# Kernel tuning notes

Hardware: AMD Instinct MI355X
Metric: run time of the kernel (lower is better)

The kernel has to match this reference:

```python
import jax, jax.numpy as jnp
import numpy as np

N, E, DIN, DOUT = 100000, 1200000, 64, 64


def setup_inputs() -> dict:
    key = jax.random.key(0)
    ks = jax.random.split(key, 6)
    x = jax.random.normal(ks[0], (N, DIN), dtype=jnp.float32)
    edge_index = jax.random.randint(ks[1], (2, E), 0, N, dtype=jnp.int32)
    edge_weight = jax.random.uniform(ks[2], (E,), dtype=jnp.float32)
    # msg_mlp: Linear(in_dim, out_dim) + ReLU
    W_msg = jax.random.normal(ks[3], (DIN, DOUT), dtype=jnp.float32) / np.sqrt(DIN)
    b_msg = jnp.zeros((DOUT,), dtype=jnp.float32)
    # update_fn (concat): Linear(in_dim + out_dim, out_dim) + ReLU
    W_upd = jax.random.normal(ks[4], (DIN + DOUT, DOUT), dtype=jnp.float32) / np.sqrt(DIN + DOUT)
    b_upd = jnp.zeros((DOUT,), dtype=jnp.float32)
    return {"x": x, "edge_index": edge_index, "edge_weight": edge_weight,
            "W_msg": W_msg, "b_msg": b_msg, "W_upd": W_upd, "b_upd": b_upd}


def reference(x, edge_index, edge_weight, W_msg, b_msg, W_upd, b_upd):
    src_idx, dst_idx = edge_index[0], edge_index[1]
    num_nodes = x.shape[0]
    # gather source node features, apply Linear+ReLU, scale by edge weight
    src_feat = x[src_idx]                                  # [E, DIN]
    msg = jax.nn.relu(src_feat @ W_msg + b_msg)            # [E, DOUT]
    msg = msg * edge_weight[:, None]
    # mean aggregation: scatter-add then divide by clamped in-degree
    agg = jax.ops.segment_sum(msg, dst_idx, num_segments=num_nodes)   # [N, DOUT]
    deg = jax.ops.segment_sum(jnp.ones((msg.shape[0],), msg.dtype), dst_idx,
                              num_segments=num_nodes)
    agg = agg / jnp.maximum(deg, 1.0)[:, None]
    # concat combine: Linear([x || agg]) + ReLU
    h = jax.nn.relu(jnp.concatenate([x, agg], axis=1) @ W_upd + b_upd)  # [N, DOUT]
    # F.normalize(p=2, dim=1), eps=1e-12
    norm = jnp.sqrt(jnp.sum(h * h, axis=1, keepdims=True))
    return h / jnp.maximum(norm, 1e-12)
```

## Files before the change

### kernel.cpp

```cpp
#include <hip/hip_runtime.h>
#include <hip/hip_fp16.h>


#define DIM 64
#define NPB 1024
#define LOG_NPB 10
#define NBUCK_MAX 128
#define CAP 16384
#define CHUNK 2048
#define EPT 8

typedef _Float16 half8 __attribute__((ext_vector_type(8)));
typedef float f32x4 __attribute__((ext_vector_type(4)));

__global__ __launch_bounds__(256) void k_mfmaA(
    const float* __restrict__ x, const float* __restrict__ Wm,
    const float* __restrict__ bm, const float* __restrict__ Wu,
    const float* __restrict__ bu, __half* __restrict__ y,
    __half* __restrict__ tq, int n) {
  int l = threadIdx.x & 63;
  int wv = threadIdx.x >> 6;
  int r = l & 15, g = l >> 4;

  half8 Bm[2][4], Bu[2][4];
#pragma unroll
  for (int ks = 0; ks < 2; ++ks)
#pragma unroll
    for (int ct = 0; ct < 4; ++ct) {
      int c = ct * 16 + r;
#pragma unroll
      for (int j = 0; j < 8; ++j) {
        int k = ks * 32 + g * 8 + j;
        Bm[ks][ct][j] = (_Float16)Wm[k * 64 + c];
        Bu[ks][ct][j] = (_Float16)Wu[k * 64 + c];
      }
    }
  float bmv[4], buv[4];
#pragma unroll
  for (int ct = 0; ct < 4; ++ct) { bmv[ct] = bm[ct * 16 + r]; buv[ct] = bu[ct * 16 + r]; }

  int ntiles = (n + 15) >> 4;
  int tile = blockIdx.x * 4 + wv;
  if (tile >= ntiles) return;
  int row0 = tile << 4;

  int arow = row0 + r; if (arow >= n) arow = n - 1;
  const float* xr = x + (size_t)arow * 64;
  half8 A[2];
#pragma unroll
  for (int ks = 0; ks < 2; ++ks) {
    float4 v0 = *(const float4*)(xr + ks * 32 + g * 8);
    float4 v1 = *(const float4*)(xr + ks * 32 + g * 8 + 4);
    A[ks][0] = (_Float16)v0.x; A[ks][1] = (_Float16)v0.y;
    A[ks][2] = (_Float16)v0.z; A[ks][3] = (_Float16)v0.w;
    A[ks][4] = (_Float16)v1.x; A[ks][5] = (_Float16)v1.y;
    A[ks][6] = (_Float16)v1.z; A[ks][7] = (_Float16)v1.w;
  }

  f32x4 Dm[4], Du[4];
#pragma unroll
  for (int ct = 0; ct < 4; ++ct)
#pragma unroll
    for (int q = 0; q < 4; ++q) { Dm[ct][q] = bmv[ct]; Du[ct][q] = buv[ct]; }

#pragma unroll
  for (int ks = 0; ks < 2; ++ks)
#pragma unroll
    for (int ct = 0; ct < 4; ++ct) {
      Dm[ct] = __builtin_amdgcn_mfma_f32_16x16x32_f16(A[ks], Bm[ks][ct], Dm[ct], 0, 0, 0);
      Du[ct] = __builtin_amdgcn_mfma_f32_16x16x32_f16(A[ks], Bu[ks][ct], Du[ct], 0, 0, 0);
    }

#pragma unroll
  for (int q = 0; q < 4; ++q) {
    int row = row0 + g * 4 + q;
    if (row < n) {
#pragma unroll
      for (int ct = 0; ct < 4; ++ct) {
        y[(size_t)row * 64 + ct * 16 + r]  = __float2half(fmaxf(Dm[ct][q], 0.0f));
        tq[(size_t)row * 64 + ct * 16 + r] = __float2half(Du[ct][q]);
      }
    }
  }
}

__global__ __launch_bounds__(256) void k_partA(
    const int* __restrict__ src, const int* __restrict__ dst,
    const float* __restrict__ ew,
    unsigned long long* __restrict__ recS, unsigned short* __restrict__ dlocS,
    int* __restrict__ bucketCur, int E, int nbuck) {
  __shared__ int hist[NBUCK_MAX];
  __shared__ int gbase[NBUCK_MAX];
  int t = threadIdx.x;
  int base = blockIdx.x * CHUNK;

  for (int b = t; b < nbuck; b += 256) hist[b] = 0;
  __syncthreads();

  unsigned long long rec[EPT];
  unsigned short dl[EPT];
  short bk[EPT];
#pragma unroll
  for (int i = 0; i < EPT; ++i) {
    int e = base + i * 256 + t;
    if (e < E) {
      int d = dst[e];
      int b = d >> LOG_NPB;
      bk[i] = (short)b;
      dl[i] = (unsigned short)(d & (NPB - 1));
      rec[i] = ((unsigned long long)__float_as_uint(ew[e]) << 32) | (unsigned)src[e];
      atomicAdd(&hist[b], 1);
    } else {
      bk[i] = -1;
    }
  }
  __syncthreads();
  for (int b = t; b < nbuck; b += 256)
    gbase[b] = atomicAdd(&bucketCur[b], hist[b]);
  __syncthreads();
  for (int b = t; b < nbuck; b += 256) hist[b] = 0;
  __syncthreads();
#pragma unroll
  for (int i = 0; i < EPT; ++i) {
    if (bk[i] >= 0) {
      int b = bk[i];
      int lp = gbase[b] + atomicAdd(&hist[b], 1);
      if (lp < CAP) {
        size_t pos = (size_t)b * CAP + lp;
        recS[pos] = rec[i];
        dlocS[pos] = dl[i];
      }
    }
  }
}

__global__ __launch_bounds__(1024) void k_partB(
    const unsigned long long* __restrict__ recS, const unsigned short* __restrict__ dlocS,
    const int* __restrict__ bucketCur,
    unsigned long long* __restrict__ sw, int* __restrict__ cnt,
    int* __restrict__ rowstart, int n) {
  __shared__ int lcnt[NPB];
  __shared__ int loff[NPB];
  __shared__ int wsum[16];
  int b = blockIdx.x;
  int t = threadIdx.x;
  int m = bucketCur[b];
  if (m > CAP) m = CAP;
  size_t sbase = (size_t)b * CAP;
  int bktbase = 0;
  for (int q = 0; q < b; ++q) bktbase += bucketCur[q];

  lcnt[t] = 0;
  __syncthreads();
  for (int i = t; i < m; i += 1024)
    atomicAdd(&lcnt[dlocS[sbase + i]], 1);
  __syncthreads();

  int v = lcnt[t];
  int lane = t & 63;
  int incl = v;
#pragma unroll
  for (int off = 1; off < 64; off <<= 1) {
    int tt = __shfl_up(incl, off, 64);
    if (lane >= off) incl += tt;
  }
  if (lane == 63) wsum[t >> 6] = incl;
  __syncthreads();
  int woff = 0;
  for (int q = 0; q < (t >> 6); ++q) woff += wsum[q];
  int excl = incl - v + woff;
  loff[t] = excl;
  int gn = (b << LOG_NPB) + t;
  if (gn < n) {
    cnt[gn] = v;
    rowstart[gn] = bktbase + excl;
  }
  __syncthreads();

  for (int i = t; i < m; i += 1024) {
    int dl = dlocS[sbase + i];
    int p = atomicAdd(&loff[dl], 1);
    sw[bktbase + p] = recS[sbase + i];
  }
}

__global__ __launch_bounds__(256) void k_gather(
    const unsigned long long* __restrict__ sw, const int* __restrict__ rowstart,
    const int* __restrict__ cnt, const __half2* __restrict__ y2,
    float* __restrict__ agg, int n) {
  int lane = threadIdx.x & 31;
  int node = (int)((blockIdx.x * (size_t)blockDim.x + threadIdx.x) >> 5);
  if (node >= n) return;
  int c = cnt[node];
  int e = rowstart[node];
  int end = e + c;
  float ax = 0.0f, ay = 0.0f;
  for (; e + 8 <= end; e += 8) {
    unsigned long long r0 = sw[e + 0];
    unsigned long long r1 = sw[e + 1];
    unsigned long long r2 = sw[e + 2];
    unsigned long long r3 = sw[e + 3];
    unsigned long long r4 = sw[e + 4];
    unsigned long long r5 = sw[e + 5];
    unsigned long long r6 = sw[e + 6];
    unsigned long long r7 = sw[e + 7];
    __half2 v0 = y2[(size_t)(unsigned)(r0 & 0xFFFFFFFFu) * 32 + lane];
    __half2 v1 = y2[(size_t)(unsigned)(r1 & 0xFFFFFFFFu) * 32 + lane];
    __half2 v2 = y2[(size_t)(unsigned)(r2 & 0xFFFFFFFFu) * 32 + lane];
    __half2 v3 = y2[(size_t)(unsigned)(r3 & 0xFFFFFFFFu) * 32 + lane];
    __half2 v4 = y2[(size_t)(unsigned)(r4 & 0xFFFFFFFFu) * 32 + lane];
    __half2 v5 = y2[(size_t)(unsigned)(r5 & 0xFFFFFFFFu) * 32 + lane];
    __half2 v6 = y2[(size_t)(unsigned)(r6 & 0xFFFFFFFFu) * 32 + lane];
    __half2 v7 = y2[(size_t)(unsigned)(r7 & 0xFFFFFFFFu) * 32 + lane];
    float w0 = __uint_as_float((unsigned)(r0 >> 32));
    float w1 = __uint_as_float((unsigned)(r1 >> 32));
    float w2 = __uint_as_float((unsigned)(r2 >> 32));
    float w3 = __uint_as_float((unsigned)(r3 >> 32));
    float w4 = __uint_as_float((unsigned)(r4 >> 32));
    float w5 = __uint_as_float((unsigned)(r5 >> 32));
    float w6 = __uint_as_float((unsigned)(r6 >> 32));
    float w7 = __uint_as_float((unsigned)(r7 >> 32));
    float2 f0 = __half22float2(v0);
    float2 f1 = __half22float2(v1);
    float2 f2 = __half22float2(v2);
    float2 f3 = __half22float2(v3);
    float2 f4 = __half22float2(v4);
    float2 f5 = __half22float2(v5);
    float2 f6 = __half22float2(v6);
    float2 f7 = __half22float2(v7);
    ax = fmaf(f0.x, w0, ax); ay = fmaf(f0.y, w0, ay);
    ax = fmaf(f1.x, w1, ax); ay = fmaf(f1.y, w1, ay);
    ax = fmaf(f2.x, w2, ax); ay = fmaf(f2.y, w2, ay);
    ax = fmaf(f3.x, w3, ax); ay = fmaf(f3.y, w3, ay);
    ax = fmaf(f4.x, w4, ax); ay = fmaf(f4.y, w4, ay);
    ax = fmaf(f5.x, w5, ax); ay = fmaf(f5.y, w5, ay);
    ax = fmaf(f6.x, w6, ax); ay = fmaf(f6.y, w6, ay);
    ax = fmaf(f7.x, w7, ax); ay = fmaf(f7.y, w7, ay);
  }
  for (; e + 4 <= end; e += 4) {
    unsigned long long r0 = sw[e + 0];
    unsigned long long r1 = sw[e + 1];
    unsigned long long r2 = sw[e + 2];
    unsigned long long r3 = sw[e + 3];
    __half2 v0 = y2[(size_t)(unsigned)(r0 & 0xFFFFFFFFu) * 32 + lane];
    __half2 v1 = y2[(size_t)(unsigned)(r1 & 0xFFFFFFFFu) * 32 + lane];
    __half2 v2 = y2[(size_t)(unsigned)(r2 & 0xFFFFFFFFu) * 32 + lane];
    __half2 v3 = y2[(size_t)(unsigned)(r3 & 0xFFFFFFFFu) * 32 + lane];
    float w0 = __uint_as_float((unsigned)(r0 >> 32));
    float w1 = __uint_as_float((unsigned)(r1 >> 32));
    float w2 = __uint_as_float((unsigned)(r2 >> 32));
    float w3 = __uint_as_float((unsigned)(r3 >> 32));
    float2 f0 = __half22float2(v0);
    float2 f1 = __half22float2(v1);
    float2 f2 = __half22float2(v2);
    float2 f3 = __half22float2(v3);
    ax = fmaf(f0.x, w0, ax); ay = fmaf(f0.y, w0, ay);
    ax = fmaf(f1.x, w1, ax); ay = fmaf(f1.y, w1, ay);
    ax = fmaf(f2.x, w2, ax); ay = fmaf(f2.y, w2, ay);
    ax = fmaf(f3.x, w3, ax); ay = fmaf(f3.y, w3, ay);
  }
  for (; e < end; ++e) {
    unsigned long long r = sw[e];
    __half2 vv = y2[(size_t)(unsigned)(r & 0xFFFFFFFFu) * 32 + lane];
    float w = __uint_as_float((unsigned)(r >> 32));
    float2 f = __half22float2(vv);
    ax = fmaf(f.x, w, ax); ay = fmaf(f.y, w, ay);
  }
  float invd = 1.0f / fmaxf((float)c, 1.0f);
  float2 o; o.x = ax * invd; o.y = ay * invd;
  *(float2*)&agg[(size_t)node * 64 + lane * 2] = o;
}

__global__ __launch_bounds__(256) void k_updB2(
    const float* __restrict__ agg ,
    const __half* __restrict__ tq, const float* __restrict__ Wu,
    float* __restrict__ out, int n) {
  int l = threadIdx.x & 63;
  int wv = threadIdx.x >> 6;
  int r = l & 15, g = l >> 4;

  half8 B2[2][4];
#pragma unroll
  for (int ks = 0; ks < 2; ++ks)
#pragma unroll
    for (int ct = 0; ct < 4; ++ct) {
      int c = ct * 16 + r;
#pragma unroll
      for (int j = 0; j < 8; ++j) {
        int k = 64 + ks * 32 + g * 8 + j;
        B2[ks][ct][j] = (_Float16)Wu[k * 64 + c];
      }
    }

  int ntiles = (n + 15) >> 4;
  int tile = blockIdx.x * 4 + wv;
  if (tile >= ntiles) return;
  int row0 = tile << 4;

  int arow = row0 + r; if (arow >= n) arow = n - 1;
  const float* ar = agg + (size_t)arow * 64;
  half8 A[2];
#pragma unroll
  for (int ks = 0; ks < 2; ++ks) {
    float4 v0 = *(const float4*)(ar + ks * 32 + g * 8);
    float4 v1 = *(const float4*)(ar + ks * 32 + g * 8 + 4);
    A[ks][0] = (_Float16)v0.x; A[ks][1] = (_Float16)v0.y;
    A[ks][2] = (_Float16)v0.z; A[ks][3] = (_Float16)v0.w;
    A[ks][4] = (_Float16)v1.x; A[ks][5] = (_Float16)v1.y;
    A[ks][6] = (_Float16)v1.z; A[ks][7] = (_Float16)v1.w;
  }

  f32x4 D[4];
#pragma unroll
  for (int ct = 0; ct < 4; ++ct)
#pragma unroll
    for (int q = 0; q < 4; ++q) {
      int row = row0 + g * 4 + q;
      D[ct][q] = (row < n) ? __half2float(tq[(size_t)row * 64 + ct * 16 + r]) : 0.0f;
    }

#pragma unroll
  for (int ks = 0; ks < 2; ++ks)
#pragma unroll
    for (int ct = 0; ct < 4; ++ct)
      D[ct] = __builtin_amdgcn_mfma_f32_16x16x32_f16(A[ks], B2[ks][ct], D[ct], 0, 0, 0);

#pragma unroll
  for (int q = 0; q < 4; ++q) {
    float h0 = fmaxf(D[0][q], 0.0f);
    float h1 = fmaxf(D[1][q], 0.0f);
    float h2 = fmaxf(D[2][q], 0.0f);
    float h3 = fmaxf(D[3][q], 0.0f);
    float ss = h0 * h0 + h1 * h1 + h2 * h2 + h3 * h3;
#pragma unroll
    for (int off = 1; off < 16; off <<= 1) ss += __shfl_xor(ss, off, 64);
    float inv = 1.0f / fmaxf(sqrtf(ss), 1e-12f);
    int row = row0 + g * 4 + q;
    if (row < n) {
      out[(size_t)row * 64 + 0 * 16 + r] = h0 * inv;
      out[(size_t)row * 64 + 1 * 16 + r] = h1 * inv;
      out[(size_t)row * 64 + 2 * 16 + r] = h2 * inv;
      out[(size_t)row * 64 + 3 * 16 + r] = h3 * inv;
    }
  }
}

extern "C" void kernel_launch(void* const* d_in, const int* in_sizes, int n_in,
                              void* d_out, int out_size, void* d_ws, size_t ws_size,
                              hipStream_t stream) {
  const float* x  = (const float*)d_in[0];
  const int*   ei = (const int*)d_in[1];
  const float* ew = (const float*)d_in[2];
  const float* Wm = (const float*)d_in[3];
  const float* bm = (const float*)d_in[4];
  const float* Wu = (const float*)d_in[5];
  const float* bu = (const float*)d_in[6];

  int n = in_sizes[0] / DIM;
  int E = in_sizes[2];
  const int* srcIdx = ei;
  const int* dstIdx = ei + E;
  int nbuck = (n + NPB - 1) >> LOG_NPB;

  __half* y = (__half*)d_ws;
  unsigned long long* sw = (unsigned long long*)(y + (size_t)n * DIM);
  unsigned long long* recS = sw + E;
  unsigned short* dlocS = (unsigned short*)(recS + (size_t)nbuck * CAP);
  int* cnt      = (int*)(dlocS + (size_t)nbuck * CAP);
  int* rowstart = cnt + n;
  int* bucketCur = rowstart + n;
  __half* tq = (__half*)recS;

  hipMemsetAsync(bucketCur, 0, NBUCK_MAX * sizeof(int), stream);

  int nblkA = (E + CHUNK - 1) / CHUNK;
  k_partA<<<nblkA, 256, 0, stream>>>(srcIdx, dstIdx, ew, recS, dlocS, bucketCur, E, nbuck);
  k_partB<<<nbuck, 1024, 0, stream>>>(recS, dlocS, bucketCur, sw, cnt, rowstart, n);

  int ntiles = (n + 15) >> 4;
  int nblkG = (ntiles + 3) / 4;
  k_mfmaA<<<nblkG, 256, 0, stream>>>(x, Wm, bm, Wu, bu, y, tq, n);
  k_gather<<<(n + 7) / 8, 256, 0, stream>>>(sw, rowstart, cnt, (const __half2*)y,
                                            (float*)d_out, n);
  k_updB2<<<nblkG, 256, 0, stream>>>((const float*)d_out, tq, Wu, (float*)d_out, n);
}
```

Measured before the change: 201.9 us.

## Pack dst-local index into edge record and gather two nodes per half-warp

The 10-bit destination-local index is packed into bits 17-26 of the 64-bit edge record, alongside a 17-bit source index. This removes the separate dlocS array and its reads and writes in both partition kernels. The gather kernel now has each 32-lane group process two nodes, interleaving their edge loads to raise memory-level parallelism, with per-node tails handled afterwards. The packing limits source indices to 17 bits (N up to 131072), which fits N=100000 but is not general.

```diff
diff --git a/kernel.cpp b/kernel.cpp
--- a/kernel.cpp
+++ b/kernel.cpp
@@ -9,6 +9,7 @@
 #define CAP 16384
 #define CHUNK 2048
 #define EPT 8
+#define SRCM 0x1FFFFu
 
 typedef _Float16 half8 __attribute__((ext_vector_type(8)));
 typedef float f32x4 __attribute__((ext_vector_type(4)));
@@ -86,8 +87,7 @@
 
 __global__ __launch_bounds__(256) void k_partA(
     const int* __restrict__ src, const int* __restrict__ dst,
-    const float* __restrict__ ew,
-    unsigned long long* __restrict__ recS, unsigned short* __restrict__ dlocS,
+    const float* __restrict__ ew, unsigned long long* __restrict__ recS,
     int* __restrict__ bucketCur, int E, int nbuck) {
   __shared__ int hist[NBUCK_MAX];
   __shared__ int gbase[NBUCK_MAX];
@@ -98,7 +98,6 @@
   __syncthreads();
 
   unsigned long long rec[EPT];
-  unsigned short dl[EPT];
   short bk[EPT];
 #pragma unroll
   for (int i = 0; i < EPT; ++i) {
@@ -107,8 +106,9 @@
       int d = dst[e];
       int b = d >> LOG_NPB;
       bk[i] = (short)b;
-      dl[i] = (unsigned short)(d & (NPB - 1));
-      rec[i] = ((unsigned long long)__float_as_uint(ew[e]) << 32) | (unsigned)src[e];
+      rec[i] = ((unsigned long long)__float_as_uint(ew[e]) << 32)
+             | ((unsigned long long)(d & (NPB - 1)) << 17)
+             | (unsigned)src[e];
       atomicAdd(&hist[b], 1);
     } else {
       bk[i] = -1;
@@ -125,18 +125,13 @@
     if (bk[i] >= 0) {
       int b = bk[i];
       int lp = gbase[b] + atomicAdd(&hist[b], 1);
-      if (lp < CAP) {
-        size_t pos = (size_t)b * CAP + lp;
-        recS[pos] = rec[i];
-        dlocS[pos] = dl[i];
-      }
+      if (lp < CAP) recS[(size_t)b * CAP + lp] = rec[i];
     }
   }
 }
 
 __global__ __launch_bounds__(1024) void k_partB(
-    const unsigned long long* __restrict__ recS, const unsigned short* __restrict__ dlocS,
-    const int* __restrict__ bucketCur,
+    const unsigned long long* __restrict__ recS, const int* __restrict__ bucketCur,
     unsigned long long* __restrict__ sw, int* __restrict__ cnt,
     int* __restrict__ rowstart, int n) {
   __shared__ int lcnt[NPB];
@@ -150,10 +145,12 @@
   int bktbase = 0;
   for (int q = 0; q < b; ++q) bktbase += bucketCur[q];
 
+  const unsigned* recLo = (const unsigned*)recS;
+
   lcnt[t] = 0;
   __syncthreads();
   for (int i = t; i < m; i += 1024)
-    atomicAdd(&lcnt[dlocS[sbase + i]], 1);
+    atomicAdd(&lcnt[(recLo[2 * (sbase + i)] >> 17) & (NPB - 1)], 1);
   __syncthreads();
 
   int v = lcnt[t];
@@ -178,97 +175,117 @@
   __syncthreads();
 
   for (int i = t; i < m; i += 1024) {
-    int dl = dlocS[sbase + i];
+    unsigned long long rec = recS[sbase + i];
+    int dl = (int)((rec >> 17) & (NPB - 1));
     int p = atomicAdd(&loff[dl], 1);
-    sw[bktbase + p] = recS[sbase + i];
-  }
-}
+    sw[bktbase + p] = rec;
+  }
+}
+
+#define YLOAD(rr) y2[(size_t)(unsigned)((rr) & SRCM) * 32 + lane]
+#define WOF(rr) __uint_as_float((unsigned)((rr) >> 32))
 
 __global__ __launch_bounds__(256) void k_gather(
     const unsigned long long* __restrict__ sw, const int* __restrict__ rowstart,
     const int* __restrict__ cnt, const __half2* __restrict__ y2,
     float* __restrict__ agg, int n) {
   int lane = threadIdx.x & 31;
-  int node = (int)((blockIdx.x * (size_t)blockDim.x + threadIdx.x) >> 5);
-  if (node >= n) return;
-  int c = cnt[node];
-  int e = rowstart[node];
-  int end = e + c;
-  float ax = 0.0f, ay = 0.0f;
-  for (; e + 8 <= end; e += 8) {
-    unsigned long long r0 = sw[e + 0];
-    unsigned long long r1 = sw[e + 1];
-    unsigned long long r2 = sw[e + 2];
-    unsigned long long r3 = sw[e + 3];
-    unsigned long long r4 = sw[e + 4];
-    unsigned long long r5 = sw[e + 5];
-    unsigned long long r6 = sw[e + 6];
-    unsigned long long r7 = sw[e + 7];
-    __half2 v0 = y2[(size_t)(unsigned)(r0 & 0xFFFFFFFFu) * 32 + lane];
-    __half2 v1 = y2[(size_t)(unsigned)(r1 & 0xFFFFFFFFu) * 32 + lane];
-    __half2 v2 = y2[(size_t)(unsigned)(r2 & 0xFFFFFFFFu) * 32 + lane];
-    __half2 v3 = y2[(size_t)(unsigned)(r3 & 0xFFFFFFFFu) * 32 + lane];
-    __half2 v4 = y2[(size_t)(unsigned)(r4 & 0xFFFFFFFFu) * 32 + lane];
-    __half2 v5 = y2[(size_t)(unsigned)(r5 & 0xFFFFFFFFu) * 32 + lane];
-    __half2 v6 = y2[(size_t)(unsigned)(r6 & 0xFFFFFFFFu) * 32 + lane];
-    __half2 v7 = y2[(size_t)(unsigned)(r7 & 0xFFFFFFFFu) * 32 + lane];
-    float w0 = __uint_as_float((unsigned)(r0 >> 32));
-    float w1 = __uint_as_float((unsigned)(r1 >> 32));
-    float w2 = __uint_as_float((unsigned)(r2 >> 32));
-    float w3 = __uint_as_float((unsigned)(r3 >> 32));
-    float w4 = __uint_as_float((unsigned)(r4 >> 32));
-    float w5 = __uint_as_float((unsigned)(r5 >> 32));
-    float w6 = __uint_as_float((unsigned)(r6 >> 32));
-    float w7 = __uint_as_float((unsigned)(r7 >> 32));
-    float2 f0 = __half22float2(v0);
-    float2 f1 = __half22float2(v1);
-    float2 f2 = __half22float2(v2);
-    float2 f3 = __half22float2(v3);
-    float2 f4 = __half22float2(v4);
-    float2 f5 = __half22float2(v5);
-    float2 f6 = __half22float2(v6);
-    float2 f7 = __half22float2(v7);
-    ax = fmaf(f0.x, w0, ax); ay = fmaf(f0.y, w0, ay);
-    ax = fmaf(f1.x, w1, ax); ay = fmaf(f1.y, w1, ay);
-    ax = fmaf(f2.x, w2, ax); ay = fmaf(f2.y, w2, ay);
-    ax = fmaf(f3.x, w3, ax); ay = fmaf(f3.y, w3, ay);
-    ax = fmaf(f4.x, w4, ax); ay = fmaf(f4.y, w4, ay);
-    ax = fmaf(f5.x, w5, ax); ay = fmaf(f5.y, w5, ay);
-    ax = fmaf(f6.x, w6, ax); ay = fmaf(f6.y, w6, ay);
-    ax = fmaf(f7.x, w7, ax); ay = fmaf(f7.y, w7, ay);
-  }
-  for (; e + 4 <= end; e += 4) {
-    unsigned long long r0 = sw[e + 0];
-    unsigned long long r1 = sw[e + 1];
-    unsigned long long r2 = sw[e + 2];
-    unsigned long long r3 = sw[e + 3];
-    __half2 v0 = y2[(size_t)(unsigned)(r0 & 0xFFFFFFFFu) * 32 + lane];
-    __half2 v1 = y2[(size_t)(unsigned)(r1 & 0xFFFFFFFFu) * 32 + lane];
-    __half2 v2 = y2[(size_t)(unsigned)(r2 & 0xFFFFFFFFu) * 32 + lane];
-    __half2 v3 = y2[(size_t)(unsigned)(r3 & 0xFFFFFFFFu) * 32 + lane];
-    float w0 = __uint_as_float((unsigned)(r0 >> 32));
-    float w1 = __uint_as_float((unsigned)(r1 >> 32));
-    float w2 = __uint_as_float((unsigned)(r2 >> 32));
-    float w3 = __uint_as_float((unsigned)(r3 >> 32));
-    float2 f0 = __half22float2(v0);
-    float2 f1 = __half22float2(v1);
-    float2 f2 = __half22float2(v2);
-    float2 f3 = __half22float2(v3);
-    ax = fmaf(f0.x, w0, ax); ay = fmaf(f0.y, w0, ay);
-    ax = fmaf(f1.x, w1, ax); ay = fmaf(f1.y, w1, ay);
-    ax = fmaf(f2.x, w2, ax); ay = fmaf(f2.y, w2, ay);
-    ax = fmaf(f3.x, w3, ax); ay = fmaf(f3.y, w3, ay);
-  }
-  for (; e < end; ++e) {
-    unsigned long long r = sw[e];
-    __half2 vv = y2[(size_t)(unsigned)(r & 0xFFFFFFFFu) * 32 + lane];
-    float w = __uint_as_float((unsigned)(r >> 32));
-    float2 f = __half22float2(vv);
-    ax = fmaf(f.x, w, ax); ay = fmaf(f.y, w, ay);
-  }
-  float invd = 1.0f / fmaxf((float)c, 1.0f);
-  float2 o; o.x = ax * invd; o.y = ay * invd;
-  *(float2*)&agg[(size_t)node * 64 + lane * 2] = o;
+  int h = (int)((blockIdx.x * (size_t)blockDim.x + threadIdx.x) >> 5);
+  int n0 = h * 2, n1 = h * 2 + 1;
+  if (n0 >= n) return;
+
+  int c0 = cnt[n0], e0 = rowstart[n0], E0 = e0 + c0;
+  float a0x = 0.0f, a0y = 0.0f, a1x = 0.0f, a1y = 0.0f;
+  int c1 = 0, e1 = 0, E1 = 0;
+  if (n1 < n) { c1 = cnt[n1]; e1 = rowstart[n1]; E1 = e1 + c1; }
+
+  while (e0 + 4 <= E0 && e1 + 4 <= E1) {
+    unsigned long long r0 = sw[e0 + 0];
+    unsigned long long r1 = sw[e0 + 1];
+    unsigned long long r2 = sw[e0 + 2];
+    unsigned long long r3 = sw[e0 + 3];
+    unsigned long long r4 = sw[e1 + 0];
+    unsigned long long r5 = sw[e1 + 1];
+    unsigned long long r6 = sw[e1 + 2];
+    unsigned long long r7 = sw[e1 + 3];
+    __half2 v0 = YLOAD(r0); __half2 v1 = YLOAD(r1);
+    __half2 v2 = YLOAD(r2); __half2 v3 = YLOAD(r3);
+    __half2 v4 = YLOAD(r4); __half2 v5 = YLOAD(r5);
+    __half2 v6 = YLOAD(r6); __half2 v7 = YLOAD(r7);
+    float w0 = WOF(r0), w1 = WOF(r1), w2 = WOF(r2), w3 = WOF(r3);
+    float w4 = WOF(r4), w5 = WOF(r5), w6 = WOF(r6), w7 = WOF(r7);
+    float2 f0 = __half22float2(v0); float2 f1 = __half22float2(v1);
+    float2 f2 = __half22float2(v2); float2 f3 = __half22float2(v3);
+    float2 f4 = __half22float2(v4); float2 f5 = __half22float2(v5);
+    float2 f6 = __half22float2(v6); float2 f7 = __half22float2(v7);
+    a0x = fmaf(f0.x, w0, a0x); a0y = fmaf(f0.y, w0, a0y);
+    a0x = fmaf(f1.x, w1, a0x); a0y = fmaf(f1.y, w1, a0y);
+    a0x = fmaf(f2.x, w2, a0x); a0y = fmaf(f2.y, w2, a0y);
+    a0x = fmaf(f3.x, w3, a0x); a0y = fmaf(f3.y, w3, a0y);
+    a1x = fmaf(f4.x, w4, a1x); a1y = fmaf(f4.y, w4, a1y);
+    a1x = fmaf(f5.x, w5, a1x); a1y = fmaf(f5.y, w5, a1y);
+    a1x = fmaf(f6.x, w6, a1x); a1y = fmaf(f6.y, w6, a1y);
+    a1x = fmaf(f7.x, w7, a1x); a1y = fmaf(f7.y, w7, a1y);
+    e0 += 4; e1 += 4;
+  }
+
+#pragma unroll
+  for (int s = 0; s < 2; ++s) {
+    int e = s ? e1 : e0;
+    int E_ = s ? E1 : E0;
+    float ax = 0.0f, ay = 0.0f;
+    for (; e + 8 <= E_; e += 8) {
+      unsigned long long r0 = sw[e + 0], r1 = sw[e + 1], r2 = sw[e + 2], r3 = sw[e + 3];
+      unsigned long long r4 = sw[e + 4], r5 = sw[e + 5], r6 = sw[e + 6], r7 = sw[e + 7];
+      __half2 v0 = YLOAD(r0); __half2 v1 = YLOAD(r1);
+      __half2 v2 = YLOAD(r2); __half2 v3 = YLOAD(r3);
+      __half2 v4 = YLOAD(r4); __half2 v5 = YLOAD(r5);
+      __half2 v6 = YLOAD(r6); __half2 v7 = YLOAD(r7);
+      float w0 = WOF(r0), w1 = WOF(r1), w2 = WOF(r2), w3 = WOF(r3);
+      float w4 = WOF(r4), w5 = WOF(r5), w6 = WOF(r6), w7 = WOF(r7);
+      float2 f0 = __half22float2(v0); float2 f1 = __half22float2(v1);
+      float2 f2 = __half22float2(v2); float2 f3 = __half22float2(v3);
+      float2 f4 = __half22float2(v4); float2 f5 = __half22float2(v5);
+      float2 f6 = __half22float2(v6); float2 f7 = __half22float2(v7);
+      ax = fmaf(f0.x, w0, ax); ay = fmaf(f0.y, w0, ay);
+      ax = fmaf(f1.x, w1, ax); ay = fmaf(f1.y, w1, ay);
+      ax = fmaf(f2.x, w2, ax); ay = fmaf(f2.y, w2, ay);
+      ax = fmaf(f3.x, w3, ax); ay = fmaf(f3.y, w3, ay);
+      ax = fmaf(f4.x, w4, ax); ay = fmaf(f4.y, w4, ay);
+      ax = fmaf(f5.x, w5, ax); ay = fmaf(f5.y, w5, ay);
+      ax = fmaf(f6.x, w6, ax); ay = fmaf(f6.y, w6, ay);
+      ax = fmaf(f7.x, w7, ax); ay = fmaf(f7.y, w7, ay);
+    }
+    for (; e + 4 <= E_; e += 4) {
+      unsigned long long r0 = sw[e + 0], r1 = sw[e + 1], r2 = sw[e + 2], r3 = sw[e + 3];
+      __half2 v0 = YLOAD(r0); __half2 v1 = YLOAD(r1);
+      __half2 v2 = YLOAD(r2); __half2 v3 = YLOAD(r3);
+      float w0 = WOF(r0), w1 = WOF(r1), w2 = WOF(r2), w3 = WOF(r3);
+      float2 f0 = __half22float2(v0); float2 f1 = __half22float2(v1);
+      float2 f2 = __half22float2(v2); float2 f3 = __half22float2(v3);
+      ax = fmaf(f0.x, w0, ax); ay = fmaf(f0.y, w0, ay);
+      ax = fmaf(f1.x, w1, ax); ay = fmaf(f1.y, w1, ay);
+      ax = fmaf(f2.x, w2, ax); ay = fmaf(f2.y, w2, ay);
+      ax = fmaf(f3.x, w3, ax); ay = fmaf(f3.y, w3, ay);
+    }
+    for (; e < E_; ++e) {
+      unsigned long long r = sw[e];
+      __half2 vv = YLOAD(r);
+      float w = WOF(r);
+      float2 f = __half22float2(vv);
+      ax = fmaf(f.x, w, ax); ay = fmaf(f.y, w, ay);
+    }
+    if (s) { a1x += ax; a1y += ay; } else { a0x += ax; a0y += ay; }
+  }
+
+  float invd0 = 1.0f / fmaxf((float)c0, 1.0f);
+  float2 o0; o0.x = a0x * invd0; o0.y = a0y * invd0;
+  *(float2*)&agg[(size_t)n0 * 64 + lane * 2] = o0;
+  if (n1 < n) {
+    float invd1 = 1.0f / fmaxf((float)c1, 1.0f);
+    float2 o1; o1.x = a1x * invd1; o1.y = a1y * invd1;
+    *(float2*)&agg[(size_t)n1 * 64 + lane * 2] = o1;
+  }
 }
 
 __global__ __launch_bounds__(256) void k_updB2(
@@ -365,8 +382,7 @@
   __half* y = (__half*)d_ws;
   unsigned long long* sw = (unsigned long long*)(y + (size_t)n * DIM);
   unsigned long long* recS = sw + E;
-  unsigned short* dlocS = (unsigned short*)(recS + (size_t)nbuck * CAP);
-  int* cnt      = (int*)(dlocS + (size_t)nbuck * CAP);
+  int* cnt      = (int*)(recS + (size_t)nbuck * CAP);
   int* rowstart = cnt + n;
   int* bucketCur = rowstart + n;
   __half* tq = (__half*)recS;
@@ -374,13 +390,14 @@
   hipMemsetAsync(bucketCur, 0, NBUCK_MAX * sizeof(int), stream);
 
   int nblkA = (E + CHUNK - 1) / CHUNK;
-  k_partA<<<nblkA, 256, 0, stream>>>(srcIdx, dstIdx, ew, recS, dlocS, bucketCur, E, nbuck);
-  k_partB<<<nbuck, 1024, 0, stream>>>(recS, dlocS, bucketCur, sw, cnt, rowstart, n);
+  k_partA<<<nblkA, 256, 0, stream>>>(srcIdx, dstIdx, ew, recS, bucketCur, E, nbuck);
+  k_partB<<<nbuck, 1024, 0, stream>>>(recS, bucketCur, sw, cnt, rowstart, n);
 
   int ntiles = (n + 15) >> 4;
   int nblkG = (ntiles + 3) / 4;
   k_mfmaA<<<nblkG, 256, 0, stream>>>(x, Wm, bm, Wu, bu, y, tq, n);
-  k_gather<<<(n + 7) / 8, 256, 0, stream>>>(sw, rowstart, cnt, (const __half2*)y,
-                                            (float*)d_out, n);
+  int nhw = (n + 1) / 2;
+  k_gather<<<(nhw + 7) / 8, 256, 0, stream>>>(sw, rowstart, cnt, (const __half2*)y,
+                                              (float*)d_out, n);
   k_updB2<<<nblkG, 256, 0, stream>>>((const float*)d_out, tq, Wu, (float*)d_out, n);
 }
```

Result: no change. 203.6 us (+0.8%).
